# Kernel tuning notes

Measured on AMD Instinct MI355X. Metric: run time of the kernel, lower is better.

Reference implementation:

```python
import jax, jax.numpy as jnp
import numpy as np

N_NODES = 50000
N_EDGES = 800000
IN_CH = 128
OUT_CH = 32
HEADS = 4
NEG_SLOPE = 0.2


def setup_inputs() -> dict:
    key = jax.random.key(0)
    k = jax.random.split(key, 6)
    x = jax.random.normal(k[0], (N_NODES, IN_CH), dtype=jnp.float32)
    edge_index = jax.random.randint(k[1], (2, N_EDGES), 0, N_NODES, dtype=jnp.int32)
    # Glorot-style init for the learned parameters of GATConv
    W = jax.random.normal(k[2], (IN_CH, HEADS * OUT_CH), dtype=jnp.float32) / np.sqrt(IN_CH)
    att_src = jax.random.normal(k[3], (HEADS, OUT_CH), dtype=jnp.float32) / np.sqrt(OUT_CH)
    att_dst = jax.random.normal(k[4], (HEADS, OUT_CH), dtype=jnp.float32) / np.sqrt(OUT_CH)
    bias = jnp.zeros((HEADS * OUT_CH,), dtype=jnp.float32)
    return {"x": x, "edge_index": edge_index, "W": W,
            "att_src": att_src, "att_dst": att_dst, "bias": bias}


def reference(x, edge_index, W, att_src, att_dst, bias):
    # PyG GATConv, single layer: concat=True, add_self_loops=True, neg_slope=0.2
    N = x.shape[0]
    H, C = att_src.shape
    # add self loops (PyG default)
    loop = jnp.arange(N, dtype=edge_index.dtype)
    src = jnp.concatenate([edge_index[0], loop])  # [E+N] message sources j
    dst = jnp.concatenate([edge_index[1], loop])  # [E+N] message targets i
    # linear projection per head
    h = (x @ W).reshape(N, H, C)                  # [N,H,C]
    a_src = jnp.einsum('nhc,hc->nh', h, att_src)  # [N,H]
    a_dst = jnp.einsum('nhc,hc->nh', h, att_dst)  # [N,H]
    # edge-wise attention logits with LeakyReLU
    e = jax.nn.leaky_relu(a_src[src] + a_dst[dst], NEG_SLOPE)  # [E',H]
    # segment softmax over incoming edges of each destination node
    m = jax.ops.segment_max(e, dst, num_segments=N)            # [N,H]
    expe = jnp.exp(e - m[dst])
    denom = jax.ops.segment_sum(expe, dst, num_segments=N)     # [N,H]
    alpha = expe / denom[dst]                                  # [E',H]
    # scatter-aggregate weighted messages
    out = jax.ops.segment_sum(h[src] * alpha[:, :, None], dst, num_segments=N)  # [N,H,C]
    return out.reshape(N, H * C) + bias
```

## Files before the change

### kernel.cpp

```cpp
#include <hip/hip_runtime.h>


constexpr int N_NODES = 50000;
constexpr int N_EDGES = 800000;
constexpr int E_TOT   = N_EDGES + N_NODES;
constexpr int HC      = 128;
constexpr float NEG_SLOPE = 0.2f;
constexpr int M_TILES = N_NODES / 16;
constexpr int NB_GEMM = 512;
constexpr int NB_HIST = 512;
constexpr int SCAN_BLOCKS = (N_NODES + 1023) / 1024;

typedef short short8 __attribute__((ext_vector_type(8)));
typedef float f32x4  __attribute__((ext_vector_type(4)));

__device__ inline unsigned short f2bf(float f) {
    unsigned int u = __float_as_uint(f);
    u += 0x7FFF + ((u >> 16) & 1);
    return (unsigned short)(u >> 16);
}


__global__ __launch_bounds__(256) void gemm_hist(
    const float* __restrict__ x,
    const float* __restrict__ W,
    const float* __restrict__ att_src, const float* __restrict__ att_dst,
    const int* __restrict__ edst,
    unsigned short* __restrict__ hb,
    float* __restrict__ a_src, float* __restrict__ a_dst,
    int* __restrict__ deg, unsigned short* __restrict__ ppos)
{
    if (blockIdx.x >= NB_GEMM) {
        const int t0 = (blockIdx.x - NB_GEMM) * 256 + threadIdx.x;
        for (int e = t0; e < N_EDGES; e += NB_HIST * 256)
            ppos[e] = (unsigned short)atomicAdd(&deg[edst[e]], 1);
        return;
    }
    const int wave = threadIdx.x >> 6;
    const int lane = threadIdx.x & 63;
    const int n0   = (wave & 1) * 64;
    const int l15  = lane & 15;
    const int quad = lane >> 4;

    short8 bfrag[4][4];
    #pragma unroll
    for (int t = 0; t < 4; ++t)
        #pragma unroll
        for (int ks = 0; ks < 4; ++ks) {
            short8 b;
            #pragma unroll
            for (int j = 0; j < 8; ++j)
                b[j] = (short)f2bf(W[(ks * 32 + quad * 8 + j) * 128 + n0 + t * 16 + l15]);
            bfrag[t][ks] = b;
        }

    float asw[4], adw[4];
    #pragma unroll
    for (int t = 0; t < 4; ++t) {
        asw[t] = att_src[n0 + t * 16 + l15];
        adw[t] = att_dst[n0 + t * 16 + l15];
    }

    for (int mt = blockIdx.x * 2 + (wave >> 1); mt < M_TILES; mt += NB_GEMM * 2) {
        const int m0 = mt * 16;
        short8 afrag[4];
        #pragma unroll
        for (int ks = 0; ks < 4; ++ks) {
            const float4 u0 = *(const float4*)&x[(size_t)(m0 + l15) * 128 + ks * 32 + quad * 8];
            const float4 u1 = *(const float4*)&x[(size_t)(m0 + l15) * 128 + ks * 32 + quad * 8 + 4];
            short8 a;
            a[0] = (short)f2bf(u0.x); a[1] = (short)f2bf(u0.y);
            a[2] = (short)f2bf(u0.z); a[3] = (short)f2bf(u0.w);
            a[4] = (short)f2bf(u1.x); a[5] = (short)f2bf(u1.y);
            a[6] = (short)f2bf(u1.z); a[7] = (short)f2bf(u1.w);
            afrag[ks] = a;
        }

        f32x4 acc[4];
        #pragma unroll
        for (int t = 0; t < 4; ++t) acc[t] = (f32x4){0.f, 0.f, 0.f, 0.f};

        #pragma unroll
        for (int ks = 0; ks < 4; ++ks)
            #pragma unroll
            for (int t = 0; t < 4; ++t)
                acc[t] = __builtin_amdgcn_mfma_f32_16x16x32_bf16(afrag[ks], bfrag[t][ks], acc[t], 0, 0, 0);

        #pragma unroll
        for (int t = 0; t < 4; ++t)
            #pragma unroll
            for (int r = 0; r < 4; ++r)
                hb[(m0 + quad * 4 + r) * 128 + n0 + t * 16 + l15] = f2bf(acc[t][r]);

        float hs[2][4] = {{0.f,0.f,0.f,0.f},{0.f,0.f,0.f,0.f}};
        float hd[2][4] = {{0.f,0.f,0.f,0.f},{0.f,0.f,0.f,0.f}};
        #pragma unroll
        for (int t = 0; t < 4; ++t)
            #pragma unroll
            for (int r = 0; r < 4; ++r) {
                hs[t >> 1][r] += acc[t][r] * asw[t];
                hd[t >> 1][r] += acc[t][r] * adw[t];
            }
        #pragma unroll
        for (int off = 1; off < 16; off <<= 1)
            #pragma unroll
            for (int g = 0; g < 2; ++g)
                #pragma unroll
                for (int r = 0; r < 4; ++r) {
                    hs[g][r] += __shfl_xor(hs[g][r], off);
                    hd[g][r] += __shfl_xor(hd[g][r], off);
                }
        if (l15 == 0) {
            const int hb0 = n0 >> 5;
            #pragma unroll
            for (int g = 0; g < 2; ++g)
                #pragma unroll
                for (int r = 0; r < 4; ++r) {
                    a_src[(m0 + quad * 4 + r) * 4 + hb0 + g] = hs[g][r];
                    a_dst[(m0 + quad * 4 + r) * 4 + hb0 + g] = hd[g][r];
                }
        }
    }
}


__global__ __launch_bounds__(256) void scan(
    const int* __restrict__ deg, int* __restrict__ partial, int* __restrict__ bsum)
{
    __shared__ int wsum[4];
    const int tid  = threadIdx.x;
    const int lane = tid & 63;
    const int wv   = tid >> 6;
    const int base = blockIdx.x * 1024 + tid * 4;
    int d0 = 0, d1 = 0, d2 = 0, d3 = 0;
    if (base + 3 < N_NODES) {
        const int4 v = *(const int4*)&deg[base];
        d0 = v.x + 1; d1 = v.y + 1; d2 = v.z + 1; d3 = v.w + 1;
    } else {
        if (base + 0 < N_NODES) d0 = deg[base + 0] + 1;
        if (base + 1 < N_NODES) d1 = deg[base + 1] + 1;
        if (base + 2 < N_NODES) d2 = deg[base + 2] + 1;
        if (base + 3 < N_NODES) d3 = deg[base + 3] + 1;
    }
    const int s0 = d0, s1 = s0 + d1, s2 = s1 + d2, s3 = s2 + d3;
    int inc = s3;
    #pragma unroll
    for (int off = 1; off < 64; off <<= 1) {
        const int t = __shfl_up(inc, off);
        if (lane >= off) inc += t;
    }
    if (lane == 63) wsum[wv] = inc;
    __syncthreads();
    int wbase = 0;
    for (int k = 0; k < wv; ++k) wbase += wsum[k];
    const int tb = wbase + inc - s3;
    if (base + 3 < N_NODES) {
        *(int4*)&partial[base] = (int4){tb, tb + s0, tb + s1, tb + s2};
    } else {
        if (base + 0 < N_NODES) partial[base + 0] = tb;
        if (base + 1 < N_NODES) partial[base + 1] = tb + s0;
        if (base + 2 < N_NODES) partial[base + 2] = tb + s1;
        if (base + 3 < N_NODES) partial[base + 3] = tb + s2;
    }
    if (tid == 255) bsum[blockIdx.x] = wbase + inc;
}


__global__ __launch_bounds__(256) void scatter_fin(
    const int* __restrict__ esrc, const int* __restrict__ edst,
    const int* __restrict__ partial, const int* __restrict__ bsum,
    const unsigned short* __restrict__ ppos,
    int* __restrict__ row_st, unsigned short* __restrict__ csr_src)
{
    __shared__ int sb[64];
    if (threadIdx.x < 64) {
        const int v = (threadIdx.x < SCAN_BLOCKS) ? bsum[threadIdx.x] : 0;
        int s = v;
        #pragma unroll
        for (int off = 1; off < 64; off <<= 1) {
            const int t = __shfl_up(s, off);
            if ((int)threadIdx.x >= off) s += t;
        }
        sb[threadIdx.x] = s - v;
    }
    __syncthreads();
    const int idx = blockIdx.x * 256 + threadIdx.x;
    if (idx < N_EDGES) {
        const int d = edst[idx];
        csr_src[partial[d] + sb[d >> 10] + 1 + ppos[idx]] = (unsigned short)esrc[idx];
    } else if (idx < E_TOT) {
        const int i = idx - N_EDGES;
        const int r = partial[i] + sb[i >> 10];
        row_st[i] = r;
        csr_src[r] = (unsigned short)i;
        if (i == 0) row_st[N_NODES] = E_TOT;
    }
}


__global__ __launch_bounds__(256) void gat_agg(
    const int* __restrict__ row_start, const unsigned short* __restrict__ csr_src,
    const unsigned short* __restrict__ hb, const float* __restrict__ a_src,
    const float* __restrict__ a_dst, const float* __restrict__ bias,
    float* __restrict__ out)
{
    __shared__ float ws[4][256];
    const int wv = threadIdx.x >> 6;
    const int node = blockIdx.x * 4 + wv;
    if (node >= N_NODES) return;
    const int lane = threadIdx.x & 63;
    const int q    = lane >> 4;
    const int li   = lane & 15;
    const int ch0  = li * 8;
    const int hd   = li >> 2;
    const float4 ad4 = *(const float4*)&a_dst[node * 4];
    const int p0 = row_start[node], p1 = row_start[node + 1];

    float acc[8] = {0.f,0.f,0.f,0.f,0.f,0.f,0.f,0.f};
    float dsum = 0.f;

    for (int base = p0; base < p1; base += 64) {
        int m = p1 - base; if (m > 64) m = 64;
        int sv = 0;
        if (lane < m) {
            sv = (int)csr_src[base + lane];
            const float4 av = *(const float4*)&a_src[sv * 4];
            float t; float4 w4;
            t = av.x + ad4.x; t = t > 0.f ? t : NEG_SLOPE * t; w4.x = __expf(t);
            t = av.y + ad4.y; t = t > 0.f ? t : NEG_SLOPE * t; w4.y = __expf(t);
            t = av.z + ad4.z; t = t > 0.f ? t : NEG_SLOPE * t; w4.z = __expf(t);
            t = av.w + ad4.w; t = t > 0.f ? t : NEG_SLOPE * t; w4.w = __expf(t);
            *(float4*)&ws[wv][lane * 4] = w4;
        }
        const int i0 = (q < m) ? q : 0;
        int s_cur = __shfl(sv, i0);
        uint4 hv = *(const uint4*)&hb[(size_t)s_cur * 128 + ch0];
        for (int j = 0; j < m; j += 4) {
            const int ei  = j + q;
            const int idx = ei < m ? ei : j;
            const int ein = ei + 4;
            const int idxn = ein < m ? ein : 0;
            const int s_nxt = __shfl(sv, idxn);
            const uint4 hvn = *(const uint4*)&hb[(size_t)s_nxt * 128 + ch0];
            float w = ws[wv][idx * 4 + hd];
            if (ei >= m) w = 0.f;
            acc[0] += w * __uint_as_float(hv.x << 16);
            acc[1] += w * __uint_as_float(hv.x & 0xFFFF0000u);
            acc[2] += w * __uint_as_float(hv.y << 16);
            acc[3] += w * __uint_as_float(hv.y & 0xFFFF0000u);
            acc[4] += w * __uint_as_float(hv.z << 16);
            acc[5] += w * __uint_as_float(hv.z & 0xFFFF0000u);
            acc[6] += w * __uint_as_float(hv.w << 16);
            acc[7] += w * __uint_as_float(hv.w & 0xFFFF0000u);
            dsum += w;
            hv = hvn;
        }
    }
    #pragma unroll
    for (int off = 16; off <= 32; off <<= 1) {
        #pragma unroll
        for (int r = 0; r < 8; ++r) acc[r] += __shfl_xor(acc[r], off);
        dsum += __shfl_xor(dsum, off);
    }
    if (q == 0) {
        const float inv = 1.f / dsum;
        const float4 b0 = *(const float4*)&bias[ch0];
        const float4 b1 = *(const float4*)&bias[ch0 + 4];
        float4 o0, o1;
        o0.x = acc[0]*inv + b0.x; o0.y = acc[1]*inv + b0.y;
        o0.z = acc[2]*inv + b0.z; o0.w = acc[3]*inv + b0.w;
        o1.x = acc[4]*inv + b1.x; o1.y = acc[5]*inv + b1.y;
        o1.z = acc[6]*inv + b1.z; o1.w = acc[7]*inv + b1.w;
        *(float4*)&out[(size_t)node * HC + ch0]     = o0;
        *(float4*)&out[(size_t)node * HC + ch0 + 4] = o1;
    }
}

extern "C" void kernel_launch(void* const* d_in, const int* in_sizes, int n_in,
                              void* d_out, int out_size, void* d_ws, size_t ws_size,
                              hipStream_t stream) {
    const float* x       = (const float*)d_in[0];
    const int*   ei      = (const int*)  d_in[1];
    const float* W       = (const float*)d_in[2];
    const float* att_src = (const float*)d_in[3];
    const float* att_dst = (const float*)d_in[4];
    const float* bias    = (const float*)d_in[5];
    float* out = (float*)d_out;

    char* p = (char*)d_ws;
    unsigned short* hb  = (unsigned short*)p; p += (size_t)N_NODES * HC * 2;
    float* a_src = (float*)p; p += (size_t)N_NODES * 4 * 4;
    float* a_dst = (float*)p; p += (size_t)N_NODES * 4 * 4;
    unsigned short* csr_src = (unsigned short*)p; p += (size_t)E_TOT * 2;
    unsigned short* ppos    = (unsigned short*)p; p += (size_t)N_EDGES * 2;
    int* partial = (int*)p;   p += N_NODES * 4;
    int* row_st  = (int*)p;   p += (N_NODES + 4) * 4;
    int* deg     = (int*)p;   p += N_NODES * 4;
    int* bsum    = (int*)p;

    const int* esrc = ei;
    const int* edst = ei + N_EDGES;

    hipMemsetAsync(deg, 0, (size_t)N_NODES * sizeof(int), stream);

    gemm_hist  <<<NB_GEMM + NB_HIST, 256, 0, stream>>>(x, W, att_src, att_dst,
                                                       edst, hb, a_src, a_dst, deg, ppos);
    scan       <<<SCAN_BLOCKS, 256, 0, stream>>>(deg, partial, bsum);
    scatter_fin<<<(E_TOT + 255) / 256, 256, 0, stream>>>(esrc, edst, partial, bsum,
                                                         ppos, row_st, csr_src);
    gat_agg    <<<(N_NODES + 3) / 4, 256, 0, stream>>>(row_st, csr_src, hb, a_src,
                                                       a_dst, bias, out);
}
```

Before: 169.1 us.

## Precompute edge attention weights during CSR scatter instead of in aggregation

The per-edge LeakyReLU and exp attention weights are now computed in the scatter kernel and written to a CSR-ordered weight array. The aggregation kernel loads them contiguously instead of gathering a_src by source index and recomputing. This moves the random a_src gather out of the latency-critical aggregation loop. The cost is an extra 13.6 MB write plus read of the weight array, and scattered float4 stores in the scatter kernel.

```diff
diff --git a/kernel.cpp b/kernel.cpp
--- a/kernel.cpp
+++ b/kernel.cpp
@@ -170,7 +170,9 @@
     const int* __restrict__ esrc, const int* __restrict__ edst,
     const int* __restrict__ partial, const int* __restrict__ bsum,
     const unsigned short* __restrict__ ppos,
-    int* __restrict__ row_st, unsigned short* __restrict__ csr_src)
+    const float* __restrict__ a_src, const float* __restrict__ a_dst,
+    int* __restrict__ row_st, unsigned short* __restrict__ csr_src,
+    float* __restrict__ wcsr)
 {
     __shared__ int sb[64];
     if (threadIdx.x < 64) {
@@ -187,12 +189,30 @@
     const int idx = blockIdx.x * 256 + threadIdx.x;
     if (idx < N_EDGES) {
         const int d = edst[idx];
-        csr_src[partial[d] + sb[d >> 10] + 1 + ppos[idx]] = (unsigned short)esrc[idx];
+        const int s = esrc[idx];
+        const int slot = partial[d] + sb[d >> 10] + 1 + ppos[idx];
+        csr_src[slot] = (unsigned short)s;
+        const float4 av = *(const float4*)&a_src[s * 4];
+        const float4 dv = *(const float4*)&a_dst[d * 4];
+        float t; float4 w4;
+        t = av.x + dv.x; t = t > 0.f ? t : NEG_SLOPE * t; w4.x = __expf(t);
+        t = av.y + dv.y; t = t > 0.f ? t : NEG_SLOPE * t; w4.y = __expf(t);
+        t = av.z + dv.z; t = t > 0.f ? t : NEG_SLOPE * t; w4.z = __expf(t);
+        t = av.w + dv.w; t = t > 0.f ? t : NEG_SLOPE * t; w4.w = __expf(t);
+        *(float4*)&wcsr[(size_t)slot * 4] = w4;
     } else if (idx < E_TOT) {
         const int i = idx - N_EDGES;
         const int r = partial[i] + sb[i >> 10];
         row_st[i] = r;
         csr_src[r] = (unsigned short)i;
+        const float4 av = *(const float4*)&a_src[i * 4];
+        const float4 dv = *(const float4*)&a_dst[i * 4];
+        float t; float4 w4;
+        t = av.x + dv.x; t = t > 0.f ? t : NEG_SLOPE * t; w4.x = __expf(t);
+        t = av.y + dv.y; t = t > 0.f ? t : NEG_SLOPE * t; w4.y = __expf(t);
+        t = av.z + dv.z; t = t > 0.f ? t : NEG_SLOPE * t; w4.z = __expf(t);
+        t = av.w + dv.w; t = t > 0.f ? t : NEG_SLOPE * t; w4.w = __expf(t);
+        *(float4*)&wcsr[(size_t)r * 4] = w4;
         if (i == 0) row_st[N_NODES] = E_TOT;
     }
 }
@@ -200,9 +220,8 @@
 
 __global__ __launch_bounds__(256) void gat_agg(
     const int* __restrict__ row_start, const unsigned short* __restrict__ csr_src,
-    const unsigned short* __restrict__ hb, const float* __restrict__ a_src,
-    const float* __restrict__ a_dst, const float* __restrict__ bias,
-    float* __restrict__ out)
+    const unsigned short* __restrict__ hb, const float* __restrict__ wcsr,
+    const float* __restrict__ bias, float* __restrict__ out)
 {
     __shared__ float ws[4][256];
     const int wv = threadIdx.x >> 6;
@@ -213,7 +232,6 @@
     const int li   = lane & 15;
     const int ch0  = li * 8;
     const int hd   = li >> 2;
-    const float4 ad4 = *(const float4*)&a_dst[node * 4];
     const int p0 = row_start[node], p1 = row_start[node + 1];
 
     float acc[8] = {0.f,0.f,0.f,0.f,0.f,0.f,0.f,0.f};
@@ -224,13 +242,7 @@
         int sv = 0;
         if (lane < m) {
             sv = (int)csr_src[base + lane];
-            const float4 av = *(const float4*)&a_src[sv * 4];
-            float t; float4 w4;
-            t = av.x + ad4.x; t = t > 0.f ? t : NEG_SLOPE * t; w4.x = __expf(t);
-            t = av.y + ad4.y; t = t > 0.f ? t : NEG_SLOPE * t; w4.y = __expf(t);
-            t = av.z + ad4.z; t = t > 0.f ? t : NEG_SLOPE * t; w4.z = __expf(t);
-            t = av.w + ad4.w; t = t > 0.f ? t : NEG_SLOPE * t; w4.w = __expf(t);
-            *(float4*)&ws[wv][lane * 4] = w4;
+            *(float4*)&ws[wv][lane * 4] = *(const float4*)&wcsr[(size_t)(base + lane) * 4];
         }
         const int i0 = (q < m) ? q : 0;
         int s_cur = __shfl(sv, i0);
@@ -291,6 +303,7 @@
     unsigned short* hb  = (unsigned short*)p; p += (size_t)N_NODES * HC * 2;
     float* a_src = (float*)p; p += (size_t)N_NODES * 4 * 4;
     float* a_dst = (float*)p; p += (size_t)N_NODES * 4 * 4;
+    float* wcsr  = (float*)p; p += (size_t)E_TOT * 4 * 4;
     unsigned short* csr_src = (unsigned short*)p; p += (size_t)E_TOT * 2;
     unsigned short* ppos    = (unsigned short*)p; p += (size_t)N_EDGES * 2;
     int* partial = (int*)p;   p += N_NODES * 4;
@@ -307,7 +320,8 @@
                                                        edst, hb, a_src, a_dst, deg, ppos);
     scan       <<<SCAN_BLOCKS, 256, 0, stream>>>(deg, partial, bsum);
     scatter_fin<<<(E_TOT + 255) / 256, 256, 0, stream>>>(esrc, edst, partial, bsum,
-                                                         ppos, row_st, csr_src);
-    gat_agg    <<<(N_NODES + 3) / 4, 256, 0, stream>>>(row_st, csr_src, hb, a_src,
-                                                       a_dst, bias, out);
-}
+                                                         ppos, a_src, a_dst,
+                                                         row_st, csr_src, wcsr);
+    gat_agg    <<<(N_NODES + 3) / 4, 256, 0, stream>>>(row_st, csr_src, hb, wcsr,
+                                                       bias, out);
+}
```

New measurement: 184.0 us. 8.8% more time.

## Process two destination nodes per wavefront in GAT aggregation

Applied to the files above, without the earlier changes.

Each wavefront now handles two consecutive destination nodes. The index, attention-logit and first feature-row loads for both nodes are issued up front, and then each node's edges are aggregated in turn. The goal is more memory-level parallelism and amortised per-node setup (row_start, bias, reductions) in the latency-bound gather. It costs more registers, which may lower occupancy, and halves the number of wavefronts launched. The two per-node loops still run sequentially, so the overlap comes only from the hoisted prologue loads.

```diff
diff --git a/kernel.cpp b/kernel.cpp
--- a/kernel.cpp
+++ b/kernel.cpp
@@ -204,75 +204,170 @@
     const float* __restrict__ a_dst, const float* __restrict__ bias,
     float* __restrict__ out)
 {
-    __shared__ float ws[4][256];
+    __shared__ float ws[4][2][256];
     const int wv = threadIdx.x >> 6;
-    const int node = blockIdx.x * 4 + wv;
-    if (node >= N_NODES) return;
+    const int nA = blockIdx.x * 8 + wv * 2;
+    if (nA >= N_NODES) return;
+    const int nB = nA + 1;
     const int lane = threadIdx.x & 63;
     const int q    = lane >> 4;
     const int li   = lane & 15;
     const int ch0  = li * 8;
     const int hd   = li >> 2;
-    const float4 ad4 = *(const float4*)&a_dst[node * 4];
-    const int p0 = row_start[node], p1 = row_start[node + 1];
-
-    float acc[8] = {0.f,0.f,0.f,0.f,0.f,0.f,0.f,0.f};
-    float dsum = 0.f;
-
-    for (int base = p0; base < p1; base += 64) {
-        int m = p1 - base; if (m > 64) m = 64;
-        int sv = 0;
-        if (lane < m) {
-            sv = (int)csr_src[base + lane];
-            const float4 av = *(const float4*)&a_src[sv * 4];
-            float t; float4 w4;
-            t = av.x + ad4.x; t = t > 0.f ? t : NEG_SLOPE * t; w4.x = __expf(t);
-            t = av.y + ad4.y; t = t > 0.f ? t : NEG_SLOPE * t; w4.y = __expf(t);
-            t = av.z + ad4.z; t = t > 0.f ? t : NEG_SLOPE * t; w4.z = __expf(t);
-            t = av.w + ad4.w; t = t > 0.f ? t : NEG_SLOPE * t; w4.w = __expf(t);
-            *(float4*)&ws[wv][lane * 4] = w4;
-        }
-        const int i0 = (q < m) ? q : 0;
-        int s_cur = __shfl(sv, i0);
-        uint4 hv = *(const uint4*)&hb[(size_t)s_cur * 128 + ch0];
-        for (int j = 0; j < m; j += 4) {
-            const int ei  = j + q;
-            const int idx = ei < m ? ei : j;
-            const int ein = ei + 4;
-            const int idxn = ein < m ? ein : 0;
-            const int s_nxt = __shfl(sv, idxn);
-            const uint4 hvn = *(const uint4*)&hb[(size_t)s_nxt * 128 + ch0];
-            float w = ws[wv][idx * 4 + hd];
-            if (ei >= m) w = 0.f;
-            acc[0] += w * __uint_as_float(hv.x << 16);
-            acc[1] += w * __uint_as_float(hv.x & 0xFFFF0000u);
-            acc[2] += w * __uint_as_float(hv.y << 16);
-            acc[3] += w * __uint_as_float(hv.y & 0xFFFF0000u);
-            acc[4] += w * __uint_as_float(hv.z << 16);
-            acc[5] += w * __uint_as_float(hv.z & 0xFFFF0000u);
-            acc[6] += w * __uint_as_float(hv.w << 16);
-            acc[7] += w * __uint_as_float(hv.w & 0xFFFF0000u);
-            dsum += w;
-            hv = hvn;
-        }
-    }
+
+    const int pA0 = row_start[nA];
+    const int pA1 = row_start[nA + 1];
+    const int pB0 = pA1;
+    const int pB1 = row_start[nA + 2];
+
+    const float4 adA = *(const float4*)&a_dst[nA * 4];
+    const float4 adB = *(const float4*)&a_dst[nB * 4];
+
+    const int mA0 = min(pA1 - pA0, 64);
+    const int mB0 = min(pB1 - pB0, 64);
+
+    int svA = 0, svB = 0;
+    if (lane < mA0) svA = (int)csr_src[pA0 + lane];
+    if (lane < mB0) svB = (int)csr_src[pB0 + lane];
+    if (lane < mA0) {
+        const float4 av = *(const float4*)&a_src[svA * 4];
+        float t; float4 w4;
+        t = av.x + adA.x; t = t > 0.f ? t : NEG_SLOPE * t; w4.x = __expf(t);
+        t = av.y + adA.y; t = t > 0.f ? t : NEG_SLOPE * t; w4.y = __expf(t);
+        t = av.z + adA.z; t = t > 0.f ? t : NEG_SLOPE * t; w4.z = __expf(t);
+        t = av.w + adA.w; t = t > 0.f ? t : NEG_SLOPE * t; w4.w = __expf(t);
+        *(float4*)&ws[wv][0][lane * 4] = w4;
+    }
+    if (lane < mB0) {
+        const float4 av = *(const float4*)&a_src[svB * 4];
+        float t; float4 w4;
+        t = av.x + adB.x; t = t > 0.f ? t : NEG_SLOPE * t; w4.x = __expf(t);
+        t = av.y + adB.y; t = t > 0.f ? t : NEG_SLOPE * t; w4.y = __expf(t);
+        t = av.z + adB.z; t = t > 0.f ? t : NEG_SLOPE * t; w4.z = __expf(t);
+        t = av.w + adB.w; t = t > 0.f ? t : NEG_SLOPE * t; w4.w = __expf(t);
+        *(float4*)&ws[wv][1][lane * 4] = w4;
+    }
+
+    const int iA0 = (q < mA0) ? q : 0;
+    uint4 hvA = *(const uint4*)&hb[(size_t)__shfl(svA, iA0) * 128 + ch0];
+    const int iB0 = (q < mB0) ? q : 0;
+    uint4 hvB = *(const uint4*)&hb[(size_t)__shfl(svB, iB0) * 128 + ch0];
+
+    float accA[8] = {0.f,0.f,0.f,0.f,0.f,0.f,0.f,0.f};
+    float accB[8] = {0.f,0.f,0.f,0.f,0.f,0.f,0.f,0.f};
+    float dsA = 0.f, dsB = 0.f;
+
+    {
+        int sv = svA; uint4 hv = hvA; int m = mA0; int base = pA0;
+        for (;;) {
+            for (int j = 0; j < m; j += 4) {
+                const int ei  = j + q;
+                const int idx = ei < m ? ei : j;
+                const int ein = ei + 4;
+                const int idxn = ein < m ? ein : 0;
+                const int s_nxt = __shfl(sv, idxn);
+                const uint4 hvn = *(const uint4*)&hb[(size_t)s_nxt * 128 + ch0];
+                float w = ws[wv][0][idx * 4 + hd];
+                if (ei >= m) w = 0.f;
+                accA[0] += w * __uint_as_float(hv.x << 16);
+                accA[1] += w * __uint_as_float(hv.x & 0xFFFF0000u);
+                accA[2] += w * __uint_as_float(hv.y << 16);
+                accA[3] += w * __uint_as_float(hv.y & 0xFFFF0000u);
+                accA[4] += w * __uint_as_float(hv.z << 16);
+                accA[5] += w * __uint_as_float(hv.z & 0xFFFF0000u);
+                accA[6] += w * __uint_as_float(hv.w << 16);
+                accA[7] += w * __uint_as_float(hv.w & 0xFFFF0000u);
+                dsA += w;
+                hv = hvn;
+            }
+            base += 64;
+            if (base >= pA1) break;
+            m = min(pA1 - base, 64);
+            sv = 0;
+            if (lane < m) {
+                sv = (int)csr_src[base + lane];
+                const float4 av = *(const float4*)&a_src[sv * 4];
+                float t; float4 w4;
+                t = av.x + adA.x; t = t > 0.f ? t : NEG_SLOPE * t; w4.x = __expf(t);
+                t = av.y + adA.y; t = t > 0.f ? t : NEG_SLOPE * t; w4.y = __expf(t);
+                t = av.z + adA.z; t = t > 0.f ? t : NEG_SLOPE * t; w4.z = __expf(t);
+                t = av.w + adA.w; t = t > 0.f ? t : NEG_SLOPE * t; w4.w = __expf(t);
+                *(float4*)&ws[wv][0][lane * 4] = w4;
+            }
+            const int i0 = (q < m) ? q : 0;
+            hv = *(const uint4*)&hb[(size_t)__shfl(sv, i0) * 128 + ch0];
+        }
+    }
+    {
+        int sv = svB; uint4 hv = hvB; int m = mB0; int base = pB0;
+        for (;;) {
+            for (int j = 0; j < m; j += 4) {
+                const int ei  = j + q;
+                const int idx = ei < m ? ei : j;
+                const int ein = ei + 4;
+                const int idxn = ein < m ? ein : 0;
+                const int s_nxt = __shfl(sv, idxn);
+                const uint4 hvn = *(const uint4*)&hb[(size_t)s_nxt * 128 + ch0];
+                float w = ws[wv][1][idx * 4 + hd];
+                if (ei >= m) w = 0.f;
+                accB[0] += w * __uint_as_float(hv.x << 16);
+                accB[1] += w * __uint_as_float(hv.x & 0xFFFF0000u);
+                accB[2] += w * __uint_as_float(hv.y << 16);
+                accB[3] += w * __uint_as_float(hv.y & 0xFFFF0000u);
+                accB[4] += w * __uint_as_float(hv.z << 16);
+                accB[5] += w * __uint_as_float(hv.z & 0xFFFF0000u);
+                accB[6] += w * __uint_as_float(hv.w << 16);
+                accB[7] += w * __uint_as_float(hv.w & 0xFFFF0000u);
+                dsB += w;
+                hv = hvn;
+            }
+            base += 64;
+            if (base >= pB1) break;
+            m = min(pB1 - base, 64);
+            sv = 0;
+            if (lane < m) {
+                sv = (int)csr_src[base + lane];
+                const float4 av = *(const float4*)&a_src[sv * 4];
+                float t; float4 w4;
+                t = av.x + adB.x; t = t > 0.f ? t : NEG_SLOPE * t; w4.x = __expf(t);
+                t = av.y + adB.y; t = t > 0.f ? t : NEG_SLOPE * t; w4.y = __expf(t);
+                t = av.z + adB.z; t = t > 0.f ? t : NEG_SLOPE * t; w4.z = __expf(t);
+                t = av.w + adB.w; t = t > 0.f ? t : NEG_SLOPE * t; w4.w = __expf(t);
+                *(float4*)&ws[wv][1][lane * 4] = w4;
+            }
+            const int i0 = (q < m) ? q : 0;
+            hv = *(const uint4*)&hb[(size_t)__shfl(sv, i0) * 128 + ch0];
+        }
+    }
+
     #pragma unroll
     for (int off = 16; off <= 32; off <<= 1) {
         #pragma unroll
-        for (int r = 0; r < 8; ++r) acc[r] += __shfl_xor(acc[r], off);
-        dsum += __shfl_xor(dsum, off);
+        for (int r = 0; r < 8; ++r) {
+            accA[r] += __shfl_xor(accA[r], off);
+            accB[r] += __shfl_xor(accB[r], off);
+        }
+        dsA += __shfl_xor(dsA, off);
+        dsB += __shfl_xor(dsB, off);
     }
     if (q == 0) {
-        const float inv = 1.f / dsum;
         const float4 b0 = *(const float4*)&bias[ch0];
         const float4 b1 = *(const float4*)&bias[ch0 + 4];
+        const float invA = 1.f / dsA;
         float4 o0, o1;
-        o0.x = acc[0]*inv + b0.x; o0.y = acc[1]*inv + b0.y;
-        o0.z = acc[2]*inv + b0.z; o0.w = acc[3]*inv + b0.w;
-        o1.x = acc[4]*inv + b1.x; o1.y = acc[5]*inv + b1.y;
-        o1.z = acc[6]*inv + b1.z; o1.w = acc[7]*inv + b1.w;
-        *(float4*)&out[(size_t)node * HC + ch0]     = o0;
-        *(float4*)&out[(size_t)node * HC + ch0 + 4] = o1;
+        o0.x = accA[0]*invA + b0.x; o0.y = accA[1]*invA + b0.y;
+        o0.z = accA[2]*invA + b0.z; o0.w = accA[3]*invA + b0.w;
+        o1.x = accA[4]*invA + b1.x; o1.y = accA[5]*invA + b1.y;
+        o1.z = accA[6]*invA + b1.z; o1.w = accA[7]*invA + b1.w;
+        *(float4*)&out[(size_t)nA * HC + ch0]     = o0;
+        *(float4*)&out[(size_t)nA * HC + ch0 + 4] = o1;
+        const float invB = 1.f / dsB;
+        o0.x = accB[0]*invB + b0.x; o0.y = accB[1]*invB + b0.y;
+        o0.z = accB[2]*invB + b0.z; o0.w = accB[3]*invB + b0.w;
+        o1.x = accB[4]*invB + b1.x; o1.y = accB[5]*invB + b1.y;
+        o1.z = accB[6]*invB + b1.z; o1.w = accB[7]*invB + b1.w;
+        *(float4*)&out[(size_t)nB * HC + ch0]     = o0;
+        *(float4*)&out[(size_t)nB * HC + ch0 + 4] = o1;
     }
 }
 
@@ -308,6 +403,6 @@
     scan       <<<SCAN_BLOCKS, 256, 0, stream>>>(deg, partial, bsum);
     scatter_fin<<<(E_TOT + 255) / 256, 256, 0, stream>>>(esrc, edst, partial, bsum,
                                                          ppos, row_st, csr_src);
-    gat_agg    <<<(N_NODES + 3) / 4, 256, 0, stream>>>(row_st, csr_src, hb, a_src,
+    gat_agg    <<<(N_NODES + 7) / 8, 256, 0, stream>>>(row_st, csr_src, hb, a_src,
                                                        a_dst, bias, out);
 }
```

Result: no change. 170.1 us (+0.6%).
